# Kernel optimization log

Hardware: AMD Instinct MI355X
Metric: run time of the kernel (lower is better)

## Reference

```python
import jax, jax.numpy as jnp
import numpy as np

VOC, EDIM, HDIM, SSZ, SDIM, SDEPTH, PAD = 32000, 256, 256, 128, 128, 2, 0
N, BSZ = 64, 32
T = 2 * N - 1  # 127
N_ACTS = 2  # push, pop


def _linear(key, out_d, in_d):
    k1, k2 = jax.random.split(key)
    return (jax.random.normal(k1, (out_d, in_d), jnp.float32) * 0.02,
            jax.random.normal(k2, (out_d,), jnp.float32) * 0.02)


def setup_inputs() -> dict:
    key = jax.random.key(0)
    ks = jax.random.split(key, 9)
    emb_W = jax.random.normal(ks[0], (VOC, EDIM), jnp.float32) * 0.02
    emb_W = emb_W.at[PAD].set(0.0)  # padding_idx row is zero in torch
    W_e2h, b_e2h = _linear(ks[1], HDIM, EDIM)
    W_s2h, b_s2h = _linear(ks[2], HDIM, SDIM * SDEPTH)
    W_h2h, b_h2h = _linear(ks[3], HDIM, HDIM)
    W_h2i, b_h2i = _linear(ks[4], N_ACTS + 1, HDIM)
    W_h2s, b_h2s = _linear(ks[5], SDIM, HDIM)
    W_s2u, b_s2u = _linear(ks[6], SDIM, SDIM * SDEPTH)
    empty_elem = jax.random.normal(ks[7], (1, SDIM), jnp.float32) * 0.02
    inputs = jax.random.randint(ks[8], (N, BSZ), 0, VOC)
    return dict(inputs=inputs, emb_W=emb_W, W_e2h=W_e2h, b_e2h=b_e2h,
                W_s2h=W_s2h, b_s2h=b_s2h, W_h2h=W_h2h, b_h2h=b_h2h,
                W_h2i=W_h2i, b_h2i=b_h2i, W_h2s=W_h2s, b_h2s=b_h2s,
                W_s2u=W_s2u, b_s2u=b_s2u, empty_elem=empty_elem)


def _srnn(inputs, emb_W, W_e2h, b_e2h, W_s2h, b_s2h, W_h2h, b_h2h,
          W_h2i, b_h2i, W_h2s, b_h2s, W_s2u, b_s2u, empty_elem):
    bsz = inputs.shape[1]
    embs = emb_W[inputs]                                        # [N, bsz, edim]
    pads = jnp.broadcast_to(emb_W[PAD], (T - N, bsz, EDIM))     # padded tail
    buf0 = jnp.concatenate([embs, pads], axis=0)                # [T, bsz, edim]
    hid0 = jnp.zeros((bsz, HDIM), jnp.float32)
    stack0 = jnp.broadcast_to(empty_elem, (bsz, SSZ, SDIM))

    def step(carry, t):
        hid, stack, buf = carry
        tops = stack[:, :SDEPTH, :].reshape(bsz, SDEPTH * SDIM)
        inp = buf[t]                                            # [bsz, edim]
        ihid = inp @ W_e2h.T + b_e2h + tops @ W_s2h.T + b_s2h
        hid = jax.nn.relu(hid @ W_h2h.T + b_h2h + ihid)
        inst = ihid @ W_h2i.T + b_h2i                           # [bsz, 3]
        act = jax.nn.softmax(inst[:, :N_ACTS], axis=-1)
        gamma = 1.0 + jnp.log1p(jnp.exp(inst[:, N_ACTS:]))      # [bsz, 1]
        a = act ** gamma
        a = a / (jnp.sum(a, axis=-1, keepdims=True) + 1e-16)    # sharpened acts
        p_push, p_pop = a[:, :1], a[:, 1:]                      # [bsz, 1]
        # buffer update: pop shifts the whole buffer down one slot along time
        buf_pop = jnp.concatenate([jnp.zeros_like(buf[:1]), buf[:-1]], axis=0)
        buf = p_push[None] * buf + p_pop[None] * buf_pop        # [1,bsz,1] bcast
        push_val = jax.nn.relu(hid @ W_h2s.T + b_h2s)           # [bsz, sdim]
        u_val = jax.nn.relu(tops @ W_s2u.T + b_s2u)             # [bsz, sdim]
        z = jnp.zeros((bsz, 1, SDIM), jnp.float32)
        # W_push (shift down by 1) as an index roll
        stack_push = jnp.concatenate([z, stack[:, :-1, :]], axis=1)
        stack_push = stack_push.at[:, 0, :].add(push_val)
        # W_pop = shift up by SDEPTH, then W_push = shift down by 1
        up = jnp.concatenate([stack[:, SDEPTH:, :],
                              jnp.zeros((bsz, SDEPTH, SDIM), jnp.float32)], axis=1)
        stack_pop = jnp.concatenate([z, up[:, :-1, :]], axis=1)
        stack_pop = stack_pop.at[:, 0, :].add(u_val)
        stack_pop = stack_pop.at[:, SSZ - SDEPTH + 1:, :].add(empty_elem[0])
        stack = p_push[:, :, None] * stack_push + p_pop[:, :, None] * stack_pop
        return (hid, stack, buf), (hid, a, stack[:, 0, :])

    (hid, stack, _), (outputs, acts, top_elems) = jax.lax.scan(
        step, (hid0, stack0, buf0), jnp.arange(T))
    return outputs, hid, stack, acts, top_elems


def reference(inputs, emb_W, W_e2h, b_e2h, W_s2h, b_s2h, W_h2h, b_h2h,
              W_h2i, b_h2i, W_h2s, b_h2s, W_s2u, b_s2u, empty_elem):
    return _srnn(inputs, emb_W, W_e2h, b_e2h, W_s2h, b_s2h, W_h2h, b_h2h,
                 W_h2i, b_h2i, W_h2s, b_h2s, W_s2u, b_s2u, empty_elem)
```

## Files before the change

kernel.cpp:

```cpp
#include <hip/hip_runtime.h>
#include <stdint.h>
#include <math.h>


#define T_STEPS 127

#define OUT_OFF   0
#define HID_OFF   1040384
#define STACK_OFF 1048576
#define ACTS_OFF  1572864
#define TE_OFF    1580992

#define WB_OFF 16384
#define E2H_OFF_U 131072

typedef _Float16 h2 __attribute__((ext_vector_type(2)));

__device__ __forceinline__ unsigned packh2(float a, float b){
  h2 v; v.x = (_Float16)a; v.y = (_Float16)b;
  return __builtin_bit_cast(unsigned, v);
}
__device__ __forceinline__ float h2loF(unsigned u){ h2 v = __builtin_bit_cast(h2,u); return (float)v.x; }
__device__ __forceinline__ float h2hiF(unsigned u){ h2 v = __builtin_bit_cast(h2,u); return (float)v.y; }

#if __has_builtin(__builtin_amdgcn_fdot2)
__device__ __forceinline__ float fdot2(unsigned a, unsigned b, float c){
  return __builtin_amdgcn_fdot2(__builtin_bit_cast(h2,a), __builtin_bit_cast(h2,b), c, false);
}
#else
__device__ __forceinline__ float fdot2(unsigned a, unsigned b, float c){
  return c + h2loF(a)*h2loF(b) + h2hiF(a)*h2hiF(b);
}
#endif

#if __has_builtin(__builtin_amdgcn_exp2f)
#define EXP2F(x) __builtin_amdgcn_exp2f(x)
#else
#define EXP2F(x) exp2f(x)
#endif
#if __has_builtin(__builtin_amdgcn_logf)
#define LOG2F(x) __builtin_amdgcn_logf(x)
#else
#define LOG2F(x) log2f(x)
#endif
#if __has_builtin(__builtin_amdgcn_rcpf)
#define RCPF(x) __builtin_amdgcn_rcpf(x)
#else
#define RCPF(x) (1.f/(x))
#endif

#define BAR() asm volatile("s_waitcnt lgkmcnt(0)\n\ts_barrier" ::: "memory")

#define CHOFF(u) (12*((u)>>3) + ((u)&7))

__global__ void prep_pack(const float* __restrict__ We2h, const float* __restrict__ Ws2h,
                          const float* __restrict__ Wh2h, const float* __restrict__ Wh2s,
                          const float* __restrict__ Ws2u, uint4* __restrict__ out4){
  int gid = blockIdx.x*256 + threadIdx.x;
  const float* src;
  if (gid < 16384){
    int i = gid >> 10, t_ = gid & 1023;
    const float* S = (t_ < 512) ? Ws2h : Wh2h;
    int r = t_ & 511, jp = r >> 2, ks = r & 3;
    int j = 2*jp + (i >> 3);
    int k0 = ks*64 + (i & 7)*8;
    src = S + j*256 + k0;
  } else if (gid < 24576){
    int l = gid - 16384;
    int i = l >> 10, t_ = l & 1023;
    const float* S = (t_ < 512) ? Wh2s : Ws2u;
    int tt = t_ & 511;
    int j  = 2*(tt >> 3) + (i >> 2);
    int k0 = (tt & 7)*32 + (i & 3)*8;
    src = S + j*256 + k0;
  } else {
    int l = gid - 24576;
    int i8 = l >> 8, j = l & 255;
    src = We2h + j*256 + i8*8;
  }
  uint4 r4;
  r4.x = packh2(src[0], src[1]); r4.y = packh2(src[2], src[3]);
  r4.z = packh2(src[4], src[5]); r4.w = packh2(src[6], src[7]);
  out4[gid] = r4;
}

__global__ void prep_e2h(const int* __restrict__ inputs, const float* __restrict__ embW,
                         const uint4* __restrict__ w04, unsigned* __restrict__ e2hpk){
  __shared__ float emb[8][256];
  int tid = threadIdx.x;
  int r2 = blockIdx.x >> 3, bg = blockIdx.x & 7;
  for (int q=0;q<8;q++){
    int rr = q >> 2, bb = q & 3;
    int tok = inputs[(2*r2+rr)*32 + bg*4+bb];
    emb[q][tid] = embW[tok*256 + tid];
  }
  __syncthreads();
  float acc[8] = {0.f,0.f,0.f,0.f,0.f,0.f,0.f,0.f};
  for (int i8=0;i8<32;i8++){
    uint4 u = w04[i8*256 + tid];
    unsigned uu[4] = {u.x,u.y,u.z,u.w};
    #pragma unroll
    for (int c=0;c<4;c++){
      float lo = h2loF(uu[c]), hi = h2hiF(uu[c]);
      int k = i8*8 + c*2;
      #pragma unroll
      for (int q=0;q<8;q++)
        acc[q] += emb[q][k]*lo + emb[q][k+1]*hi;
    }
  }
  int base = (bg*4)*8192 + r2*256 + tid;
  #pragma unroll
  for (int bb=0;bb<4;bb++)
    e2hpk[base + bb*8192] = packh2(acc[bb], acc[4+bb]);
}

__global__ __attribute__((amdgpu_flat_work_group_size(1024,1024), amdgpu_waves_per_eu(4,4)))
void srnn_main(const uint4* __restrict__ ws4, const unsigned* __restrict__ wsu,
               const float* __restrict__ b_e2h, const float* __restrict__ b_s2h,
               const float* __restrict__ b_h2h, const float* __restrict__ Wh2i,
               const float* __restrict__ b_h2i, const float* __restrict__ b_h2s,
               const float* __restrict__ b_s2u, const float* __restrict__ empty_el,
               float* __restrict__ out)
{
  __shared__ __align__(16) float    stk_s[128*128];
  __shared__ __align__(16) unsigned e2h_s[32*258];
  __shared__ __align__(16) unsigned s_pk[192];
  __shared__ __align__(16) unsigned hid_pk[192];
  __shared__ __align__(16) float    pv_s[128], uv_s[128];
  __shared__ __align__(16) float    accih[256], acchp[256];
  __shared__ __align__(16) float    emptyf_s[128];
  __shared__ __align__(16) float    whi_s[768];
  __shared__ float    wbuf[2][192];
  __shared__ unsigned pkwc[32];
  __shared__ float    pp_s, pq_s;

  const int tid = threadIdx.x;
  const int b   = blockIdx.x;
  const int aside = tid >> 9;
  const int ar  = tid & 511;
  const int ajp = ar >> 2;
  const int aks = ar & 3;
  const int pB  = tid >> 3;
  const int kB  = tid & 7;
  const int g   = tid >> 6;
  const int cp  = tid & 63;

  uint4 w1r[16], wBr[8];
  #pragma unroll
  for (int i=0;i<16;i++) w1r[i] = ws4[i*1024 + tid];
  #pragma unroll
  for (int i=0;i<8;i++)  wBr[i] = ws4[WB_OFF + i*1024 + tid];

  float bA0=0.f, bA1=0.f;
  if (aks==0){
    int j0 = 2*ajp;
    if (aside==0){ bA0 = b_e2h[j0]+b_s2h[j0]; bA1 = b_e2h[j0+1]+b_s2h[j0+1]; }
    else         { bA0 = b_h2h[j0];           bA1 = b_h2h[j0+1]; }
  }
  float bB0=0.f, bB1=0.f;
  if (kB==0){
    if (pB < 64){ bB0 = b_h2s[2*pB];      bB1 = b_h2s[2*pB+1]; }
    else        { bB0 = b_s2u[2*(pB-64)]; bB1 = b_s2u[2*(pB-64)+1]; }
  }
  const float bi0=b_h2i[0], bi1=b_h2i[1], bi2=b_h2i[2];

  const unsigned* e2hg = wsu + E2H_OFF_U + b*8192;
  #pragma unroll
  for (int q=0;q<8;q++){
    int idx = q*1024 + tid;
    e2h_s[(idx>>8)*258 + (idx&255)] = e2hg[idx];
  }
  {
    float2 e2 = *(const float2*)&empty_el[2*cp];
    #pragma unroll
    for (int j=0;j<8;j++)
      *(float2*)&stk_s[(8*g+j)*128 + 2*cp] = e2;
  }
  if (tid < 128){
    emptyf_s[tid] = empty_el[tid];
    hid_pk[CHOFF(tid)] = 0u;
    int cu = tid & 63;
    s_pk[CHOFF(tid)] = packh2(empty_el[2*cu], empty_el[2*cu+1]);
  }
  if (tid < 768) whi_s[tid] = Wh2i[tid];
  if (tid < 192){ wbuf[0][tid] = (tid==64)?1.f:0.f; wbuf[1][tid]=0.f; }
  if (tid < 32)  pkwc[tid] = (tid==0)? packh2(1.f,0.f) : 0u;
  __syncthreads();

  int cur = 0;
  for (int t=0;t<T_STEPS;++t){
    {
      const unsigned* act  = aside ? hid_pk : s_pk;
      const unsigned* actB = act + 48*aks;
      float x0 = 0.f, x1 = 0.f;
      if (aside==0){
        #pragma unroll
        for (int q=0;q<8;q++){
          int r2 = aks*8 + q;
          unsigned cw = pkwc[r2];
          uint2 e = *(const uint2*)&e2h_s[r2*258 + 2*ajp];
          x0 = fdot2(cw, e.x, x0);
          x1 = fdot2(cw, e.y, x1);
        }
      }
      #pragma unroll
      for (int i=0;i<8;i++){
        uint4 A  = *(const uint4*)(actB + 12*(i>>1) + 4*(i&1));
        uint4 Wa = w1r[i], Wb = w1r[8+i];
        x0 = fdot2(A.x,Wa.x,x0); x0 = fdot2(A.y,Wa.y,x0);
        x0 = fdot2(A.z,Wa.z,x0); x0 = fdot2(A.w,Wa.w,x0);
        x1 = fdot2(A.x,Wb.x,x1); x1 = fdot2(A.y,Wb.y,x1);
        x1 = fdot2(A.z,Wb.z,x1); x1 = fdot2(A.w,Wb.w,x1);
      }
      x0 += __shfl_xor(x0,1); x0 += __shfl_xor(x0,2);
      x1 += __shfl_xor(x1,1); x1 += __shfl_xor(x1,2);
      if (aks==0){
        float* dst = aside ? acchp : accih;
        *(float2*)&dst[2*ajp] = make_float2(x0 + bA0, x1 + bA1);
      }
    }
    BAR();

    if (tid < 64){
      float4 av = *(const float4*)&accih[4*tid];
      float4 q0 = *(const float4*)&whi_s[      4*tid];
      float4 q1 = *(const float4*)&whi_s[256 + 4*tid];
      float4 q2 = *(const float4*)&whi_s[512 + 4*tid];
      float p0 = av.x*q0.x + av.y*q0.y + av.z*q0.z + av.w*q0.w;
      float p1 = av.x*q1.x + av.y*q1.y + av.z*q1.z + av.w*q1.w;
      float p2 = av.x*q2.x + av.y*q2.y + av.z*q2.z + av.w*q2.w;
      #pragma unroll
      for (int o=1;o<=32;o<<=1){
        p0 += __shfl_xor(p0,o); p1 += __shfl_xor(p1,o); p2 += __shfl_xor(p2,o);
      }
      if (tid==0){
        float i0 = bi0+p0, i1 = bi1+p1, gi = bi2+p2;
        float gamma = 1.f + 0.6931471806f*LOG2F(1.f + EXP2F(1.442695041f*gi));
        float z = 1.442695041f*gamma*(i0 - i1);
        float ppv = RCPF(1.f + EXP2F(-z));
        float pqv = 1.f - ppv;
        pp_s = ppv; pq_s = pqv;
        *(float2*)&out[ACTS_OFF + t*64 + b*2] = make_float2(ppv,pqv);
      }
    }
    if (tid >= 64 && tid < 192){
      int hl = tid - 64;
      float2 ih2 = *(const float2*)&accih[2*hl];
      float2 hp2 = *(const float2*)&acchp[2*hl];
      float hn0 = fmaxf(ih2.x+hp2.x, 0.f);
      float hn1 = fmaxf(ih2.y+hp2.y, 0.f);
      hid_pk[CHOFF(hl)] = packh2(hn0,hn1);
      *(float2*)&out[OUT_OFF + t*8192 + b*256 + 2*hl] = make_float2(hn0,hn1);
      if (t==T_STEPS-1) *(float2*)&out[HID_OFF + b*256 + 2*hl] = make_float2(hn0,hn1);
    }
    BAR();

    {
      const unsigned* srcB = (pB < 64) ? hid_pk : s_pk;
      const uint4* cA0 = (const uint4*)(srcB + 24*kB);
      const uint4* cA1 = (const uint4*)(srcB + 24*kB + 12);
      uint4 A0 = cA0[0], A1 = cA0[1];
      uint4 A2 = cA1[0], A3 = cA1[1];
      float y0=0.f, y1=0.f;
      y0=fdot2(A0.x,wBr[0].x,y0); y0=fdot2(A0.y,wBr[0].y,y0); y0=fdot2(A0.z,wBr[0].z,y0); y0=fdot2(A0.w,wBr[0].w,y0);
      y0=fdot2(A1.x,wBr[1].x,y0); y0=fdot2(A1.y,wBr[1].y,y0); y0=fdot2(A1.z,wBr[1].z,y0); y0=fdot2(A1.w,wBr[1].w,y0);
      y0=fdot2(A2.x,wBr[2].x,y0); y0=fdot2(A2.y,wBr[2].y,y0); y0=fdot2(A2.z,wBr[2].z,y0); y0=fdot2(A2.w,wBr[2].w,y0);
      y0=fdot2(A3.x,wBr[3].x,y0); y0=fdot2(A3.y,wBr[3].y,y0); y0=fdot2(A3.z,wBr[3].z,y0); y0=fdot2(A3.w,wBr[3].w,y0);
      y1=fdot2(A0.x,wBr[4].x,y1); y1=fdot2(A0.y,wBr[4].y,y1); y1=fdot2(A0.z,wBr[4].z,y1); y1=fdot2(A0.w,wBr[4].w,y1);
      y1=fdot2(A1.x,wBr[5].x,y1); y1=fdot2(A1.y,wBr[5].y,y1); y1=fdot2(A1.z,wBr[5].z,y1); y1=fdot2(A1.w,wBr[5].w,y1);
      y1=fdot2(A2.x,wBr[6].x,y1); y1=fdot2(A2.y,wBr[6].y,y1); y1=fdot2(A2.z,wBr[6].z,y1); y1=fdot2(A2.w,wBr[6].w,y1);
      y1=fdot2(A3.x,wBr[7].x,y1); y1=fdot2(A3.y,wBr[7].y,y1); y1=fdot2(A3.z,wBr[7].z,y1); y1=fdot2(A3.w,wBr[7].w,y1);
      y0 += __shfl_xor(y0,1); y0 += __shfl_xor(y0,2); y0 += __shfl_xor(y0,4);
      y1 += __shfl_xor(y1,1); y1 += __shfl_xor(y1,2); y1 += __shfl_xor(y1,4);
      if (kB==0){
        float v0 = fmaxf(y0+bB0,0.f), v1 = fmaxf(y1+bB1,0.f);
        if (pB < 64) *(float2*)&pv_s[2*pB]      = make_float2(v0,v1);
        else         *(float2*)&uv_s[2*(pB-64)] = make_float2(v0,v1);
      }
    }
    BAR();
    const float pp = pp_s, pq = pq_s;

    {
      float2 w[10];
      #pragma unroll
      for (int k=0;k<10;k++){
        int r = 8*g - 1 + k;
        if (r >= 0 && r <= 127)
          w[k] = *(const float2*)&stk_s[r*128 + 2*cp];
      }
      if (g == 15) w[9] = *(const float2*)&emptyf_s[2*cp];
      float2 pv2 = make_float2(0.f,0.f), uv2 = make_float2(0.f,0.f);
      if (g == 0){ pv2 = *(const float2*)&pv_s[2*cp]; uv2 = *(const float2*)&uv_s[2*cp]; }
      float2 nn[8];
      #pragma unroll
      for (int j=0;j<8;j++){
        nn[j].x = pp*w[j].x + pq*w[j+2].x;
        nn[j].y = pp*w[j].y + pq*w[j+2].y;
      }
      if (g == 0){
        nn[0].x = pp*pv2.x + pq*uv2.x;
        nn[0].y = pp*pv2.y + pq*uv2.y;
      }
      if (tid < 128){
        int k = 64+tid;
        wbuf[cur^1][k] = pp*wbuf[cur][k] + pq*wbuf[cur][k-1];
      } else if (tid < 160){
        int r2 = tid-128;
        int k1 = 65 + t - 2*r2;
        float wa = wbuf[cur][k1], wb2 = wbuf[cur][k1-1], wc2 = wbuf[cur][k1-2];
        pkwc[r2] = packh2(pp*wa+pq*wb2, pp*wb2+pq*wc2);
      }
      BAR();
      #pragma unroll
      for (int j=0;j<8;j++)
        *(float2*)&stk_s[(8*g+j)*128 + 2*cp] = nn[j];
      if (g == 0){
        *(float2*)&out[TE_OFF + t*4096 + b*128 + 2*cp] = nn[0];
        s_pk[CHOFF(cp)]      = packh2(nn[0].x, nn[0].y);
        s_pk[CHOFF(64+cp)]   = packh2(nn[1].x, nn[1].y);
      }
    }
    BAR();
    cur ^= 1;
  }

  #pragma unroll
  for (int j=0;j<8;j++){
    int r = 8*g + j;
    *(float2*)&out[STACK_OFF + b*16384 + r*128 + 2*cp] =
      *(const float2*)&stk_s[r*128 + 2*cp];
  }
}

extern "C" void kernel_launch(void* const* d_in, const int* in_sizes, int n_in,
                              void* d_out, int out_size, void* d_ws, size_t ws_size,
                              hipStream_t stream){
  const int*   inputs = (const int*)d_in[0];
  const float* embW   = (const float*)d_in[1];
  const float* We2h   = (const float*)d_in[2];
  const float* b_e2h  = (const float*)d_in[3];
  const float* Ws2h   = (const float*)d_in[4];
  const float* b_s2h  = (const float*)d_in[5];
  const float* Wh2h   = (const float*)d_in[6];
  const float* b_h2h  = (const float*)d_in[7];
  const float* Wh2i   = (const float*)d_in[8];
  const float* b_h2i  = (const float*)d_in[9];
  const float* Wh2s   = (const float*)d_in[10];
  const float* b_h2s  = (const float*)d_in[11];
  const float* Ws2u   = (const float*)d_in[12];
  const float* b_s2u  = (const float*)d_in[13];
  const float* empty  = (const float*)d_in[14];
  unsigned* wsu = (unsigned*)d_ws;

  prep_pack<<<dim3(128), dim3(256), 0, stream>>>(We2h, Ws2h, Wh2h, Wh2s, Ws2u, (uint4*)wsu);
  prep_e2h<<<dim3(256), dim3(256), 0, stream>>>(inputs, embW, ((const uint4*)wsu)+24576, wsu + E2H_OFF_U);
  srnn_main<<<dim3(32), dim3(1024), 0, stream>>>((const uint4*)wsu, (const unsigned*)wsu,
                                                 b_e2h, b_s2h, b_h2h, Wh2i, b_h2i,
                                                 b_h2s, b_s2u, empty, (float*)d_out);
}
```

Before: 843.2 us.

## Keep stack rows in registers with double-buffered halo exchange

The 128x128 stack state now lives in per-thread registers (8 rows each) instead of a full shared-memory array. Only the boundary rows of each 8-row group are published to double-buffered halo arrays in LDS. This removes one block barrier per time step and most of the LDS reads and writes for the stack update. In exchange it uses more registers in a kernel already pinned to 1024 threads and 4 waves per EU, which risks spills.

```diff
diff --git a/kernel.cpp b/kernel.cpp
--- a/kernel.cpp
+++ b/kernel.cpp
@@ -122,13 +122,13 @@
                const float* __restrict__ b_s2u, const float* __restrict__ empty_el,
                float* __restrict__ out)
 {
-  __shared__ __align__(16) float    stk_s[128*128];
   __shared__ __align__(16) unsigned e2h_s[32*258];
+  __shared__ __align__(16) float    halo_top[2][16*128];
+  __shared__ __align__(16) float    halo_bot[2][16*128];
   __shared__ __align__(16) unsigned s_pk[192];
   __shared__ __align__(16) unsigned hid_pk[192];
   __shared__ __align__(16) float    pv_s[128], uv_s[128];
   __shared__ __align__(16) float    accih[256], acchp[256];
-  __shared__ __align__(16) float    emptyf_s[128];
   __shared__ __align__(16) float    whi_s[768];
   __shared__ float    wbuf[2][192];
   __shared__ unsigned pkwc[32];
@@ -170,14 +170,13 @@
     int idx = q*1024 + tid;
     e2h_s[(idx>>8)*258 + (idx&255)] = e2hg[idx];
   }
-  {
-    float2 e2 = *(const float2*)&empty_el[2*cp];
-    #pragma unroll
-    for (int j=0;j<8;j++)
-      *(float2*)&stk_s[(8*g+j)*128 + 2*cp] = e2;
-  }
+  const float2 emt2 = *(const float2*)&empty_el[2*cp];
+  float2 stk[8];
+  #pragma unroll
+  for (int j=0;j<8;j++) stk[j] = emt2;
+  *(float2*)&halo_top[0][g*128 + 2*cp] = emt2;
+  *(float2*)&halo_bot[0][g*128 + 2*cp] = emt2;
   if (tid < 128){
-    emptyf_s[tid] = empty_el[tid];
     hid_pk[CHOFF(tid)] = 0u;
     int cu = tid & 63;
     s_pk[CHOFF(tid)] = packh2(empty_el[2*cu], empty_el[2*cu+1]);
@@ -282,25 +281,33 @@
     const float pp = pp_s, pq = pq_s;
 
     {
-      float2 w[10];
-      #pragma unroll
-      for (int k=0;k<10;k++){
-        int r = 8*g - 1 + k;
-        if (r >= 0 && r <= 127)
-          w[k] = *(const float2*)&stk_s[r*128 + 2*cp];
-      }
-      if (g == 15) w[9] = *(const float2*)&emptyf_s[2*cp];
+      float2 wm1 = make_float2(0.f,0.f), wp8 = emt2;
+      if (g > 0)  wm1 = *(const float2*)&halo_bot[cur][(g-1)*128 + 2*cp];
+      if (g < 15) wp8 = *(const float2*)&halo_top[cur][(g+1)*128 + 2*cp];
       float2 pv2 = make_float2(0.f,0.f), uv2 = make_float2(0.f,0.f);
       if (g == 0){ pv2 = *(const float2*)&pv_s[2*cp]; uv2 = *(const float2*)&uv_s[2*cp]; }
+
       float2 nn[8];
-      #pragma unroll
-      for (int j=0;j<8;j++){
-        nn[j].x = pp*w[j].x + pq*w[j+2].x;
-        nn[j].y = pp*w[j].y + pq*w[j+2].y;
-      }
+      nn[0].x = pp*wm1.x + pq*stk[1].x;  nn[0].y = pp*wm1.y + pq*stk[1].y;
+      #pragma unroll
+      for (int j=1;j<7;j++){
+        nn[j].x = pp*stk[j-1].x + pq*stk[j+1].x;
+        nn[j].y = pp*stk[j-1].y + pq*stk[j+1].y;
+      }
+      nn[7].x = pp*stk[6].x + pq*wp8.x;  nn[7].y = pp*stk[6].y + pq*wp8.y;
       if (g == 0){
         nn[0].x = pp*pv2.x + pq*uv2.x;
         nn[0].y = pp*pv2.y + pq*uv2.y;
+      }
+      #pragma unroll
+      for (int j=0;j<8;j++) stk[j] = nn[j];
+      *(float2*)&halo_top[cur^1][g*128 + 2*cp] = nn[0];
+      *(float2*)&halo_bot[cur^1][g*128 + 2*cp] = nn[7];
+
+      if (g == 0){
+        *(float2*)&out[TE_OFF + t*4096 + b*128 + 2*cp] = nn[0];
+        s_pk[CHOFF(cp)]      = packh2(nn[0].x, nn[0].y);
+        s_pk[CHOFF(64+cp)]   = packh2(nn[1].x, nn[1].y);
       }
       if (tid < 128){
         int k = 64+tid;
@@ -311,15 +318,6 @@
         float wa = wbuf[cur][k1], wb2 = wbuf[cur][k1-1], wc2 = wbuf[cur][k1-2];
         pkwc[r2] = packh2(pp*wa+pq*wb2, pp*wb2+pq*wc2);
       }
-      BAR();
-      #pragma unroll
-      for (int j=0;j<8;j++)
-        *(float2*)&stk_s[(8*g+j)*128 + 2*cp] = nn[j];
-      if (g == 0){
-        *(float2*)&out[TE_OFF + t*4096 + b*128 + 2*cp] = nn[0];
-        s_pk[CHOFF(cp)]      = packh2(nn[0].x, nn[0].y);
-        s_pk[CHOFF(64+cp)]   = packh2(nn[1].x, nn[1].y);
-      }
     }
     BAR();
     cur ^= 1;
@@ -328,8 +326,7 @@
   #pragma unroll
   for (int j=0;j<8;j++){
     int r = 8*g + j;
-    *(float2*)&out[STACK_OFF + b*16384 + r*128 + 2*cp] =
-      *(const float2*)&stk_s[r*128 + 2*cp];
+    *(float2*)&out[STACK_OFF + b*16384 + r*128 + 2*cp] = stk[j];
   }
 }
 
```

Result: slower. 917.9 us (+8.9%).

## Use double-buffered halo rows to drop a barrier in the stack update

Applied to the files above, without the earlier changes.

Each wave now updates a 4-row slab of the stack in place using float4 accesses. Neighbouring boundary rows are exchanged through double-buffered halo arrays, so the barrier between reading the old stack and writing the new one can be removed. The packed control-weight reads in the e2h phase are also vectorised into two uint4 loads. This adds shared memory for the halo buffers and extra halo stores, and correctness depends on the halo double-buffer indexing being exact.

```diff
diff --git a/kernel.cpp b/kernel.cpp
--- a/kernel.cpp
+++ b/kernel.cpp
@@ -124,14 +124,16 @@
 {
   __shared__ __align__(16) float    stk_s[128*128];
   __shared__ __align__(16) unsigned e2h_s[32*258];
+  __shared__ __align__(16) float    halo_top[2][16*128];
+  __shared__ __align__(16) float    halo_bot[2][16*128];
   __shared__ __align__(16) unsigned s_pk[192];
   __shared__ __align__(16) unsigned hid_pk[192];
   __shared__ __align__(16) float    pv_s[128], uv_s[128];
   __shared__ __align__(16) float    accih[256], acchp[256];
   __shared__ __align__(16) float    emptyf_s[128];
   __shared__ __align__(16) float    whi_s[768];
-  __shared__ float    wbuf[2][192];
-  __shared__ unsigned pkwc[32];
+  __shared__ __align__(16) float    wbuf[2][192];
+  __shared__ __align__(16) unsigned pkwc[32];
   __shared__ float    pp_s, pq_s;
 
   const int tid = threadIdx.x;
@@ -144,6 +146,8 @@
   const int kB  = tid & 7;
   const int g   = tid >> 6;
   const int cp  = tid & 63;
+  const int sub = (tid >> 5) & 1;
+  const int c4  = tid & 31;
 
   uint4 w1r[16], wBr[8];
   #pragma unroll
@@ -175,6 +179,8 @@
     #pragma unroll
     for (int j=0;j<8;j++)
       *(float2*)&stk_s[(8*g+j)*128 + 2*cp] = e2;
+    *(float2*)&halo_top[0][g*128 + 2*cp] = e2;
+    *(float2*)&halo_bot[0][g*128 + 2*cp] = e2;
   }
   if (tid < 128){
     emptyf_s[tid] = empty_el[tid];
@@ -194,10 +200,13 @@
       const unsigned* actB = act + 48*aks;
       float x0 = 0.f, x1 = 0.f;
       if (aside==0){
+        uint4 cwa = *(const uint4*)&pkwc[8*aks];
+        uint4 cwb = *(const uint4*)&pkwc[8*aks+4];
+        unsigned cwv[8] = {cwa.x,cwa.y,cwa.z,cwa.w,cwb.x,cwb.y,cwb.z,cwb.w};
         #pragma unroll
         for (int q=0;q<8;q++){
           int r2 = aks*8 + q;
-          unsigned cw = pkwc[r2];
+          unsigned cw = cwv[q];
           uint2 e = *(const uint2*)&e2h_s[r2*258 + 2*ajp];
           x0 = fdot2(cw, e.x, x0);
           x1 = fdot2(cw, e.y, x1);
@@ -282,25 +291,48 @@
     const float pp = pp_s, pq = pq_s;
 
     {
-      float2 w[10];
-      #pragma unroll
-      for (int k=0;k<10;k++){
-        int r = 8*g - 1 + k;
-        if (r >= 0 && r <= 127)
-          w[k] = *(const float2*)&stk_s[r*128 + 2*cp];
-      }
-      if (g == 15) w[9] = *(const float2*)&emptyf_s[2*cp];
-      float2 pv2 = make_float2(0.f,0.f), uv2 = make_float2(0.f,0.f);
-      if (g == 0){ pv2 = *(const float2*)&pv_s[2*cp]; uv2 = *(const float2*)&uv_s[2*cp]; }
-      float2 nn[8];
-      #pragma unroll
-      for (int j=0;j<8;j++){
-        nn[j].x = pp*w[j].x + pq*w[j+2].x;
-        nn[j].y = pp*w[j].y + pq*w[j+2].y;
-      }
-      if (g == 0){
-        nn[0].x = pp*pv2.x + pq*uv2.x;
-        nn[0].y = pp*pv2.y + pq*uv2.y;
+      const int R = 8*g + 4*sub;
+      float4 o0, o1, o2, o3, o4, o5;
+      o1 = *(const float4*)&stk_s[(R  )*128 + 4*c4];
+      o2 = *(const float4*)&stk_s[(R+1)*128 + 4*c4];
+      o3 = *(const float4*)&stk_s[(R+2)*128 + 4*c4];
+      o4 = *(const float4*)&stk_s[(R+3)*128 + 4*c4];
+      if (sub == 0){
+        o0 = (g>0) ? *(const float4*)&halo_bot[cur][(g-1)*128 + 4*c4]
+                   : make_float4(0.f,0.f,0.f,0.f);
+        o5 = *(const float4*)&stk_s[(R+4)*128 + 4*c4];
+      } else {
+        o0 = *(const float4*)&stk_s[(R-1)*128 + 4*c4];
+        o5 = (g<15) ? *(const float4*)&halo_top[cur][(g+1)*128 + 4*c4]
+                    : *(const float4*)&emptyf_s[4*c4];
+      }
+      float4 n0, n1, n2, n3;
+      n0.x = pp*o0.x + pq*o2.x; n0.y = pp*o0.y + pq*o2.y;
+      n0.z = pp*o0.z + pq*o2.z; n0.w = pp*o0.w + pq*o2.w;
+      n1.x = pp*o1.x + pq*o3.x; n1.y = pp*o1.y + pq*o3.y;
+      n1.z = pp*o1.z + pq*o3.z; n1.w = pp*o1.w + pq*o3.w;
+      n2.x = pp*o2.x + pq*o4.x; n2.y = pp*o2.y + pq*o4.y;
+      n2.z = pp*o2.z + pq*o4.z; n2.w = pp*o2.w + pq*o4.w;
+      n3.x = pp*o3.x + pq*o5.x; n3.y = pp*o3.y + pq*o5.y;
+      n3.z = pp*o3.z + pq*o5.z; n3.w = pp*o3.w + pq*o5.w;
+      if (g == 0 && sub == 0){
+        float4 pv4 = *(const float4*)&pv_s[4*c4];
+        float4 uv4 = *(const float4*)&uv_s[4*c4];
+        n0.x = pp*pv4.x + pq*uv4.x; n0.y = pp*pv4.y + pq*uv4.y;
+        n0.z = pp*pv4.z + pq*uv4.z; n0.w = pp*pv4.w + pq*uv4.w;
+      }
+      *(float4*)&stk_s[(R  )*128 + 4*c4] = n0;
+      *(float4*)&stk_s[(R+1)*128 + 4*c4] = n1;
+      *(float4*)&stk_s[(R+2)*128 + 4*c4] = n2;
+      *(float4*)&stk_s[(R+3)*128 + 4*c4] = n3;
+      if (sub == 0) *(float4*)&halo_top[cur^1][g*128 + 4*c4] = n0;
+      else          *(float4*)&halo_bot[cur^1][g*128 + 4*c4] = n3;
+      if (g == 0 && sub == 0){
+        *(float4*)&out[TE_OFF + t*4096 + b*128 + 4*c4] = n0;
+        s_pk[CHOFF(2*c4)]      = packh2(n0.x, n0.y);
+        s_pk[CHOFF(2*c4+1)]    = packh2(n0.z, n0.w);
+        s_pk[CHOFF(64+2*c4)]   = packh2(n1.x, n1.y);
+        s_pk[CHOFF(64+2*c4+1)] = packh2(n1.z, n1.w);
       }
       if (tid < 128){
         int k = 64+tid;
@@ -311,25 +343,18 @@
         float wa = wbuf[cur][k1], wb2 = wbuf[cur][k1-1], wc2 = wbuf[cur][k1-2];
         pkwc[r2] = packh2(pp*wa+pq*wb2, pp*wb2+pq*wc2);
       }
-      BAR();
-      #pragma unroll
-      for (int j=0;j<8;j++)
-        *(float2*)&stk_s[(8*g+j)*128 + 2*cp] = nn[j];
-      if (g == 0){
-        *(float2*)&out[TE_OFF + t*4096 + b*128 + 2*cp] = nn[0];
-        s_pk[CHOFF(cp)]      = packh2(nn[0].x, nn[0].y);
-        s_pk[CHOFF(64+cp)]   = packh2(nn[1].x, nn[1].y);
-      }
     }
     BAR();
     cur ^= 1;
   }
 
-  #pragma unroll
-  for (int j=0;j<8;j++){
-    int r = 8*g + j;
-    *(float2*)&out[STACK_OFF + b*16384 + r*128 + 2*cp] =
-      *(const float2*)&stk_s[r*128 + 2*cp];
+  {
+    const int R = 8*g + 4*sub;
+    #pragma unroll
+    for (int j=0;j<4;j++){
+      *(float4*)&out[STACK_OFF + b*16384 + (R+j)*128 + 4*c4] =
+        *(const float4*)&stk_s[(R+j)*128 + 4*c4];
+    }
   }
 }
 
```

Result: no change. 828.5 us (-1.7%).
